# Performance work log

Hardware: AMD Instinct MI355X
Metric: run time of the kernel (lower is better)

## Reference

```python
import jax, jax.numpy as jnp
import numpy as np

N_E = 1024
E_DIM = 64
BETA = 0.25


def setup_inputs() -> dict:
    key = jax.random.key(0)
    k1, k2 = jax.random.split(key)
    z = jax.random.normal(k1, (32, E_DIM, 32, 32), dtype=jnp.float32)
    embedding = jax.random.uniform(k2, (N_E, E_DIM), dtype=jnp.float32,
                                   minval=-1.0 / N_E, maxval=1.0 / N_E)
    return {"z": z, "embedding": embedding}


def reference(z, embedding):
    beta = BETA
    bt, ch, h, w = z.shape
    n_e = embedding.shape[0]
    # BCHW -> BHWC, flatten to [N, e_dim]
    zp = jnp.transpose(z, (0, 2, 3, 1))
    zf = zp.reshape(-1, ch)
    # squared L2 distances to each codebook entry: [N, n_e]
    d = (jnp.sum(zf ** 2, axis=1, keepdims=True)
         + jnp.sum(embedding ** 2, axis=1)
         - 2.0 * jnp.matmul(zf, embedding.T))
    idx = jnp.argmin(d, axis=1)                      # [N]
    min_encodings = jax.nn.one_hot(idx, n_e, dtype=jnp.float32)  # [N, n_e]
    # gather codebook rows (equivalent to one_hot @ embedding)
    z_q = embedding[idx].reshape(zp.shape)           # [B,H,W,C]
    loss = (jnp.mean((jax.lax.stop_gradient(z_q) - zp) ** 2)
            + beta * jnp.mean((z_q - jax.lax.stop_gradient(zp)) ** 2))
    # straight-through estimator
    z_q_st = zp + jax.lax.stop_gradient(z_q - zp)
    e_mean = jnp.mean(min_encodings, axis=0)
    perplexity = jnp.exp(-jnp.sum(e_mean * jnp.log(e_mean + 1e-10)))
    z_q_out = jnp.transpose(z_q_st, (0, 3, 1, 2))    # back to BCHW
    min_encoding_indices = idx.reshape(bt, h, w)
    return loss, z_q_out, perplexity, min_encodings, min_encoding_indices
```

## Files before the change

kernel.cpp:

```cpp
#include <hip/hip_runtime.h>
#include <cfloat>
#include <cstddef>


#define NROWS 32768
#define NE    1024
#define EDIM  64
#define TPB_A 512
#define GRID_A 512
#define TPB_B 256
#define GRID_B 512
#define NPART 512

#define OFF_LOSS ((size_t)0)
#define OFF_ZQ   ((size_t)1)
#define OFF_PERP ((size_t)2097153)
#define OFF_OH   ((size_t)2097154)
#define OFF_IDX  ((size_t)35651586)

typedef float v2f __attribute__((ext_vector_type(2)));


__global__ __launch_bounds__(128) void vq_e2(const float* __restrict__ emb,
                                             float* __restrict__ e2buf) {
    int j = blockIdx.x * 128 + threadIdx.x;
    const float* e = emb + ((size_t)j << 6);
    double s = 0.0;
#pragma unroll
    for (int c = 0; c < EDIM; ++c) { float v = e[c]; s += (double)v * (double)v; }
    e2buf[j] = (float)s;
}

__global__ __launch_bounds__(TPB_A, 4) void vq_scan(const float* __restrict__ z,
                                                    const float* __restrict__ emb,
                                                    const float* __restrict__ e2buf,
                                                    float* __restrict__ out) {
    const int t    = threadIdx.x;
    const int lane = t & 63;
    const int q    = t >> 6;
    const int rb   = blockIdx.x >> 2;
    const int cb   = blockIdx.x & 3;
    const int r0   = rb << 8;
    const int rg   = q & 3;
    const int hf   = __builtin_amdgcn_readfirstlane(q >> 2);

    const int row  = r0 + (rg << 6) + lane;
    const int b    = row >> 10;
    const int m    = row & 1023;
    const size_t zbase = (size_t)b * 65536 + (size_t)m;

    v2f zp[32];
    double sd = 0.0;
#pragma unroll
    for (int n = 0; n < 32; ++n) {
        float x = z[zbase + (size_t)(2 * n) * 1024];
        float y = z[zbase + (size_t)(2 * n + 1) * 1024];
        zp[n] = (v2f){x, y};
        sd += (double)x * (double)x;
        sd += (double)y * (double)y;
    }
    const float z2f = (float)sd;

    {
        float* basep = out + OFF_OH + (size_t)r0 * 1024 + (cb << 8);
        for (int i = t; i < 32768; i += TPB_A) {
            int r  = i >> 7;
            int c2 = i & 127;
            *(float2*)(basep + (size_t)r * 1024 + 2 * c2) = make_float2(0.f, 0.f);
        }
    }

    const int jf = (cb << 8) + (hf << 7);
    float bestd = FLT_MAX;
    int   bestj = 0;
    for (int jj = 0; jj < 128; ++jj) {
        const int j = jf + jj;
        const float4* ep = (const float4*)(emb + ((size_t)j << 6));
        const float e2f = e2buf[j];
        float4 e[16];
#pragma unroll
        for (int k = 0; k < 16; ++k) e[k] = ep[k];
        v2f a01 = {0.f, 0.f}, a23 = {0.f, 0.f};
#pragma unroll
        for (int k = 0; k < 16; ++k) {
            v2f exy = {e[k].x, e[k].y};
            v2f ezw = {e[k].z, e[k].w};
            a01 = __builtin_elementwise_fma(exy, zp[2 * k],     a01);
            a23 = __builtin_elementwise_fma(ezw, zp[2 * k + 1], a23);
        }
        float dot = (a01.x + a01.y) + (a23.x + a23.y);
        float d   = (z2f + e2f) - 2.0f * dot;
        if (d < bestd) { bestd = d; bestj = j; }
        if ((jj & 31) == 31) __builtin_amdgcn_s_barrier();
    }

    const int gc = (cb << 1) + hf;
    out[OFF_ZQ + zbase + (size_t)(2 * gc) * 1024]     = bestd;
    out[OFF_ZQ + zbase + (size_t)(2 * gc + 1) * 1024] = __int_as_float(bestj);
}

__global__ __launch_bounds__(TPB_B) void vq_epi(const float* __restrict__ z,
                                                const float* __restrict__ emb,
                                                int* __restrict__ hist,
                                                float* __restrict__ partial,
                                                float* __restrict__ out) {
    const int t    = threadIdx.x;
    const int lane = t & 63;
    const int q    = t >> 6;
    const int r0   = blockIdx.x << 6;

    __shared__ int   s_idx[64];
    __shared__ float s_l[8];

    if (t < 64) {
        const int row = r0 + t;
        const int b   = row >> 10;
        const int m   = row & 1023;
        const size_t zbase = (size_t)b * 65536 + (size_t)m;
        const float* cp = out + OFF_ZQ + zbase;
        float bd = cp[0];
        int   bj = __float_as_int(cp[1024]);
#pragma unroll
        for (int gc = 1; gc < 8; ++gc) {
            float d = cp[(size_t)(2 * gc) * 1024];
            int   j = __float_as_int(cp[(size_t)(2 * gc + 1) * 1024]);
            if (d < bd) { bd = d; bj = j; }
        }
        s_idx[t] = bj;
        out[OFF_IDX + row] = (float)bj;
        out[OFF_OH + (size_t)row * 1024 + bj] = 1.0f;
        atomicAdd(&hist[bj], 1);
    }
    __syncthreads();

    {
        const int row = r0 + lane;
        const int b   = row >> 10;
        const int m   = row & 1023;
        const size_t zbr = (size_t)b * 65536 + (size_t)m;
        const int    jjx = s_idx[lane];
        const float* er  = emb + ((size_t)jjx << 6);
        float* zq = out + OFF_ZQ + zbr;
#pragma unroll
        for (int p = 0; p < 2; ++p) {
            const int cls = q + 4 * p;
            float ls = 0.f;
#pragma unroll
            for (int i = 0; i < 8; ++i) {
                int c = cls + 8 * i;
                float zc   = z[zbr + (size_t)c * 1024];
                float ev   = er[c];
                float diff = ev - zc;
                zq[(size_t)c * 1024] = zc + diff;
                ls = fmaf(diff, diff, ls);
            }
#pragma unroll
            for (int off = 32; off >= 1; off >>= 1) ls += __shfl_down(ls, off);
            if (lane == 0) s_l[cls] = ls;
        }
        __syncthreads();
        if (t == 0) {
            float l = 0.f;
#pragma unroll
            for (int c = 0; c < 8; ++c) l += s_l[c];
            partial[blockIdx.x] = l;
        }
    }
}

__global__ __launch_bounds__(1024) void vq_final(const int* __restrict__ hist,
                                                 const float* __restrict__ partial,
                                                 float* __restrict__ out) {
    int t = threadIdx.x;
    float p    = (float)hist[t] * (1.0f / 32768.0f);
    float term = p * logf(p + 1e-10f);
    float lp   = (t < NPART) ? partial[t] : 0.f;
#pragma unroll
    for (int off = 32; off >= 1; off >>= 1) {
        term += __shfl_down(term, off);
        lp   += __shfl_down(lp, off);
    }
    __shared__ float st[16], sl[16];
    int w = t >> 6, ln = t & 63;
    if (ln == 0) { st[w] = term; sl[w] = lp; }
    __syncthreads();
    if (t == 0) {
        float s = 0.f, l = 0.f;
#pragma unroll
        for (int i = 0; i < 16; ++i) { s += st[i]; l += sl[i]; }
        out[OFF_LOSS] = 1.25f * l * (1.0f / 2097152.0f);
        out[OFF_PERP] = expf(-s);
    }
}

extern "C" void kernel_launch(void* const* d_in, const int* in_sizes, int n_in,
                              void* d_out, int out_size, void* d_ws, size_t ws_size,
                              hipStream_t stream) {
    const float* z   = (const float*)d_in[0];
    const float* emb = (const float*)d_in[1];
    float* out     = (float*)d_out;
    int*   hist    = (int*)d_ws;
    float* partial = (float*)((char*)d_ws + 4096);
    float* e2buf   = (float*)((char*)d_ws + 8192);

    hipMemsetAsync(hist, 0, 4096, stream);
    vq_e2<<<8, 128, 0, stream>>>(emb, e2buf);
    vq_scan<<<GRID_A, TPB_A, 0, stream>>>(z, emb, e2buf, out);
    vq_epi<<<GRID_B, TPB_B, 0, stream>>>(z, emb, hist, partial, out);
    vq_final<<<1, 1024, 0, stream>>>(hist, partial, out);
}
```

Measured before the change: 226.4 us.

## Split codebook scan across four waves per block with LDS argmin merge

The scan kernel now uses 256-thread blocks covering 64 rows, where each of the four wavefronts scans a 64-entry slice of the block's 256-code chunk. The four per-wave minima are merged in shared memory, and one candidate per column-block is written, so the epilogue reduces 4 candidates instead of 8. The zeroing of the one-hot output is interleaved into the scan loop instead of run as a separate prologue, and the periodic barriers are removed. This gives more blocks and occupancy (launch bounds 5) and overlaps stores with compute, at the cost of more z reloads per row, since each row is now read by 4 blocks instead of 4 half-blocks.

```diff
diff --git a/kernel.cpp b/kernel.cpp
--- a/kernel.cpp
+++ b/kernel.cpp
@@ -6,8 +6,8 @@
 #define NROWS 32768
 #define NE    1024
 #define EDIM  64
-#define TPB_A 512
-#define GRID_A 512
+#define TPB_A 256
+#define GRID_A 2048
 #define TPB_B 256
 #define GRID_B 512
 #define NPART 512
@@ -31,7 +31,7 @@
     e2buf[j] = (float)s;
 }
 
-__global__ __launch_bounds__(TPB_A, 4) void vq_scan(const float* __restrict__ z,
+__global__ __launch_bounds__(TPB_A, 5) void vq_scan(const float* __restrict__ z,
                                                     const float* __restrict__ emb,
                                                     const float* __restrict__ e2buf,
                                                     float* __restrict__ out) {
@@ -40,14 +40,16 @@
     const int q    = t >> 6;
     const int rb   = blockIdx.x >> 2;
     const int cb   = blockIdx.x & 3;
-    const int r0   = rb << 8;
-    const int rg   = q & 3;
-    const int hf   = __builtin_amdgcn_readfirstlane(q >> 2);
-
-    const int row  = r0 + (rg << 6) + lane;
+    const int r0   = rb << 6;
+    const int qu   = __builtin_amdgcn_readfirstlane(q);
+
+    const int row  = r0 + lane;
     const int b    = row >> 10;
     const int m    = row & 1023;
     const size_t zbase = (size_t)b * 65536 + (size_t)m;
+
+    __shared__ float s_wd[4][64];
+    __shared__ int   s_wj[4][64];
 
     v2f zp[32];
     double sd = 0.0;
@@ -61,19 +63,18 @@
     }
     const float z2f = (float)sd;
 
-    {
-        float* basep = out + OFF_OH + (size_t)r0 * 1024 + (cb << 8);
-        for (int i = t; i < 32768; i += TPB_A) {
+    float* ohb = out + OFF_OH + (size_t)r0 * 1024 + (cb << 8);
+
+    const int jf = (cb << 8) + (qu << 6);
+    float bestd = FLT_MAX;
+    int   bestj = 0;
+    for (int jj = 0; jj < 64; ++jj) {
+        if (!(jj & 1)) {
+            int i  = t + (jj >> 1) * TPB_A;
             int r  = i >> 7;
             int c2 = i & 127;
-            *(float2*)(basep + (size_t)r * 1024 + 2 * c2) = make_float2(0.f, 0.f);
-        }
-    }
-
-    const int jf = (cb << 8) + (hf << 7);
-    float bestd = FLT_MAX;
-    int   bestj = 0;
-    for (int jj = 0; jj < 128; ++jj) {
+            *(float2*)(ohb + (size_t)r * 1024 + 2 * c2) = make_float2(0.f, 0.f);
+        }
         const int j = jf + jj;
         const float4* ep = (const float4*)(emb + ((size_t)j << 6));
         const float e2f = e2buf[j];
@@ -91,12 +92,24 @@
         float dot = (a01.x + a01.y) + (a23.x + a23.y);
         float d   = (z2f + e2f) - 2.0f * dot;
         if (d < bestd) { bestd = d; bestj = j; }
-        if ((jj & 31) == 31) __builtin_amdgcn_s_barrier();
-    }
-
-    const int gc = (cb << 1) + hf;
-    out[OFF_ZQ + zbase + (size_t)(2 * gc) * 1024]     = bestd;
-    out[OFF_ZQ + zbase + (size_t)(2 * gc + 1) * 1024] = __int_as_float(bestj);
+    }
+
+    s_wd[q][lane] = bestd;
+    s_wj[q][lane] = bestj;
+    __syncthreads();
+    if (t < 64) {
+        float bd = s_wd[0][t];
+        int   bj = s_wj[0][t];
+#pragma unroll
+        for (int w = 1; w < 4; ++w) {
+            float dw = s_wd[w][t];
+            if (dw < bd) { bd = dw; bj = s_wj[w][t]; }
+        }
+        const int rr = r0 + t;
+        const size_t zb2 = (size_t)(rr >> 10) * 65536 + (size_t)(rr & 1023);
+        out[OFF_ZQ + zb2 + (size_t)(2 * cb) * 1024]     = bd;
+        out[OFF_ZQ + zb2 + (size_t)(2 * cb + 1) * 1024] = __int_as_float(bj);
+    }
 }
 
 __global__ __launch_bounds__(TPB_B) void vq_epi(const float* __restrict__ z,
@@ -121,7 +134,7 @@
         float bd = cp[0];
         int   bj = __float_as_int(cp[1024]);
 #pragma unroll
-        for (int gc = 1; gc < 8; ++gc) {
+        for (int gc = 1; gc < 4; ++gc) {
             float d = cp[(size_t)(2 * gc) * 1024];
             int   j = __float_as_int(cp[(size_t)(2 * gc + 1) * 1024]);
             if (d < bd) { bd = d; bj = j; }
```

Result: faster. 211.3 us (-6.7%).

## Feed codebook via scalar registers into packed FMA and regrid scan blocks

Applied to the files above, without the earlier changes.

The scan kernel now has each block cover 512 rows against a 128-entry codebook slice, with 8 column blocks, so every wave in a block reads the same codebook entry. That wave-uniform entry is loaded into scalar registers (u64 pairs) and used directly as an SGPR operand of inline-asm v_pk_fma_f32, removing per-lane vector loads of the codebook. The histogram zeroing is folded into the e2 kernel, dropping a separate memset. The risk is that inline asm and the scalar-load path may constrain scheduling, and per-block z reads and one-hot zeroing work are redistributed.

```diff
diff --git a/kernel.cpp b/kernel.cpp
--- a/kernel.cpp
+++ b/kernel.cpp
@@ -19,11 +19,14 @@
 #define OFF_IDX  ((size_t)35651586)
 
 typedef float v2f __attribute__((ext_vector_type(2)));
+typedef unsigned long long u64;
 
 
 __global__ __launch_bounds__(128) void vq_e2(const float* __restrict__ emb,
-                                             float* __restrict__ e2buf) {
+                                             float* __restrict__ e2buf,
+                                             int* __restrict__ hist) {
     int j = blockIdx.x * 128 + threadIdx.x;
+    hist[j] = 0;
     const float* e = emb + ((size_t)j << 6);
     double s = 0.0;
 #pragma unroll
@@ -38,13 +41,11 @@
     const int t    = threadIdx.x;
     const int lane = t & 63;
     const int q    = t >> 6;
-    const int rb   = blockIdx.x >> 2;
-    const int cb   = blockIdx.x & 3;
-    const int r0   = rb << 8;
-    const int rg   = q & 3;
-    const int hf   = __builtin_amdgcn_readfirstlane(q >> 2);
-
-    const int row  = r0 + (rg << 6) + lane;
+    const int rb   = blockIdx.x >> 3;
+    const int cb   = blockIdx.x & 7;
+    const int r0   = rb << 9;
+
+    const int row  = r0 + (q << 6) + lane;
     const int b    = row >> 10;
     const int m    = row & 1023;
     const size_t zbase = (size_t)b * 65536 + (size_t)m;
@@ -62,41 +63,40 @@
     const float z2f = (float)sd;
 
     {
-        float* basep = out + OFF_OH + (size_t)r0 * 1024 + (cb << 8);
+        float* basep = out + OFF_OH + (size_t)r0 * 1024 + (cb << 7);
         for (int i = t; i < 32768; i += TPB_A) {
-            int r  = i >> 7;
-            int c2 = i & 127;
+            int r  = i >> 6;
+            int c2 = i & 63;
             *(float2*)(basep + (size_t)r * 1024 + 2 * c2) = make_float2(0.f, 0.f);
         }
     }
 
-    const int jf = (cb << 8) + (hf << 7);
+    const int jf = cb << 7;
     float bestd = FLT_MAX;
-    int   bestj = 0;
+    int   bestj = NE;
     for (int jj = 0; jj < 128; ++jj) {
         const int j = jf + jj;
-        const float4* ep = (const float4*)(emb + ((size_t)j << 6));
+        const u64* ep = (const u64*)(emb + ((size_t)j << 6));
         const float e2f = e2buf[j];
-        float4 e[16];
-#pragma unroll
-        for (int k = 0; k < 16; ++k) e[k] = ep[k];
-        v2f a01 = {0.f, 0.f}, a23 = {0.f, 0.f};
+        u64 es[32];
+#pragma unroll
+        for (int k = 0; k < 32; ++k) es[k] = ep[k];
+        v2f accA = {0.f, 0.f}, accB = {0.f, 0.f};
 #pragma unroll
         for (int k = 0; k < 16; ++k) {
-            v2f exy = {e[k].x, e[k].y};
-            v2f ezw = {e[k].z, e[k].w};
-            a01 = __builtin_elementwise_fma(exy, zp[2 * k],     a01);
-            a23 = __builtin_elementwise_fma(ezw, zp[2 * k + 1], a23);
-        }
-        float dot = (a01.x + a01.y) + (a23.x + a23.y);
+            asm("v_pk_fma_f32 %0, %1, %2, %0"
+                : "+v"(accA) : "s"(es[2 * k]), "v"(zp[2 * k]));
+            asm("v_pk_fma_f32 %0, %1, %2, %0"
+                : "+v"(accB) : "s"(es[2 * k + 1]), "v"(zp[2 * k + 1]));
+        }
+        float dot = (accA.x + accA.y) + (accB.x + accB.y);
         float d   = (z2f + e2f) - 2.0f * dot;
         if (d < bestd) { bestd = d; bestj = j; }
         if ((jj & 31) == 31) __builtin_amdgcn_s_barrier();
     }
 
-    const int gc = (cb << 1) + hf;
-    out[OFF_ZQ + zbase + (size_t)(2 * gc) * 1024]     = bestd;
-    out[OFF_ZQ + zbase + (size_t)(2 * gc + 1) * 1024] = __int_as_float(bestj);
+    out[OFF_ZQ + zbase + (size_t)(2 * cb) * 1024]     = bestd;
+    out[OFF_ZQ + zbase + (size_t)(2 * cb + 1) * 1024] = __int_as_float(bestj);
 }
 
 __global__ __launch_bounds__(TPB_B) void vq_epi(const float* __restrict__ z,
@@ -203,8 +203,7 @@
     float* partial = (float*)((char*)d_ws + 4096);
     float* e2buf   = (float*)((char*)d_ws + 8192);
 
-    hipMemsetAsync(hist, 0, 4096, stream);
-    vq_e2<<<8, 128, 0, stream>>>(emb, e2buf);
+    vq_e2<<<8, 128, 0, stream>>>(emb, e2buf, hist);
     vq_scan<<<GRID_A, TPB_A, 0, stream>>>(z, emb, e2buf, out);
     vq_epi<<<GRID_B, TPB_B, 0, stream>>>(z, emb, hist, partial, out);
     vq_final<<<1, 1024, 0, stream>>>(hist, partial, out);
```

New measurement: 231.6 us. 1.02x slower.
